# Kernel tuning notes

Hardware: AMD Instinct MI355X
Metric: run time of the kernel (lower is better)

## Reference

```python
import jax, jax.numpy as jnp
import numpy as np

B, C_IN, H, W = 32, 128, 64, 64
C_OUT, K, STRIDE, PAD = 128, 3, 1, 1
M, G = 2, 2
RC = max(C_IN // 16, 16)          # reduction channels = 16
MO = M * C_OUT                    # 256
GRP = G * C_OUT                   # fc groups = 256
OPG = (C_OUT * C_IN * K * K) // GRP   # 576 outputs per fc group
IPG = MO // GRP                   # 1 input per fc group
EPS = 1e-5


def setup_inputs() -> dict:
    key = jax.random.key(0)
    ks = jax.random.split(key, 12)
    s = 0.02
    return {
        "x": jax.random.normal(ks[0], (B, C_IN, H, W), jnp.float32),
        "mask_w": jax.random.normal(ks[1], (1, C_IN), jnp.float32) * s,
        "mask_b": jnp.zeros((1,), jnp.float32),
        "t1_w": jax.random.normal(ks[2], (RC, C_IN), jnp.float32) * s,
        "t1_b": jnp.zeros((RC,), jnp.float32),
        "ln_g": jnp.ones((RC,), jnp.float32),
        "ln_b": jnp.zeros((RC,), jnp.float32),
        "t2_w": jax.random.normal(ks[3], (MO, RC), jnp.float32) * s,
        "t2_b": jnp.zeros((MO,), jnp.float32),
        "fc_w": jax.random.normal(ks[4], (GRP, OPG, IPG), jnp.float32) * s,
        "fc_b": jnp.zeros((GRP * OPG,), jnp.float32),
    }


def reference(x, mask_w, mask_b, t1_w, t1_b, ln_g, ln_b, t2_w, t2_b, fc_w, fc_b):
    b, c, h, w = x.shape
    # --- GC attention context pooling ---
    logits = jnp.einsum('bchw,oc->bohw', x, mask_w) + mask_b[None, :, None, None]
    attn = jax.nn.softmax(logits.reshape(b, h * w), axis=-1)  # [b, hw]
    context = jnp.einsum('bchw,bs->bc', x, attn.reshape(b, h * w)) if False else \
        jnp.einsum('bcs,bs->bc', x.reshape(b, c, h * w), attn)
    # --- transform: conv1x1 -> LayerNorm -> ReLU -> conv1x1 ---
    t = jnp.einsum('bc,rc->br', context, t1_w) + t1_b
    mu = jnp.mean(t, axis=-1, keepdims=True)
    var = jnp.mean((t - mu) ** 2, axis=-1, keepdims=True)
    t = (t - mu) * jax.lax.rsqrt(var + EPS) * ln_g + ln_b
    t = jax.nn.relu(t)
    xw = jnp.einsum('br,or->bo', t, t2_w) + t2_b          # [b, M*out]
    xw = jax.nn.sigmoid(xw)
    # --- grouped 1x1 fc: generates per-sample conv weights ---
    xg = xw.reshape(b, GRP, IPG)
    gen = jnp.einsum('goi,bgi->bgo', fc_w, xg) + fc_b.reshape(GRP, OPG)
    w_gen = gen.reshape(b, C_OUT, C_IN, K, K)             # per-sample kernels
    # --- per-sample conv (groups=b trick in torch) ---
    def conv_one(xi, wi):
        return jax.lax.conv_general_dilated(
            xi[None], wi, (STRIDE, STRIDE), [(PAD, PAD), (PAD, PAD)],
            dimension_numbers=('NCHW', 'OIHW', 'NCHW'))[0]
    out = jax.vmap(conv_one)(x, w_gen)                    # [b, out, h, w]
    return out
```

## Files before the change

### kernel.cpp

```cpp
#include <hip/hip_runtime.h>
#include <hip/hip_bf16.h>

typedef unsigned short u16;
typedef unsigned int u32;
typedef __attribute__((ext_vector_type(8))) short bf16x8;
typedef __attribute__((ext_vector_type(16))) float f32x16;
typedef __attribute__((ext_vector_type(4))) int int4v;
typedef __attribute__((ext_vector_type(4))) float f32x4;

#define CIN 128
#define COUT 128
#define HWSZ 4096
#define RC 16
#define EPS 1e-5f

__device__ __forceinline__ float b2f(u16 u) {
    u32 v = ((u32)u) << 16;
    union { u32 i; float f; } c; c.i = v; return c.f;
}

__device__ __forceinline__ void dma16(const void* g, void* l) {
    __builtin_amdgcn_global_load_lds((const __attribute__((address_space(1))) void*)g,
                                     (__attribute__((address_space(3))) void*)l, 16, 0, 0);
}

__global__ __launch_bounds__(256) void k_xform(const float* __restrict__ x,
                                               const float* __restrict__ mask_w,
                                               const float* __restrict__ mask_b,
                                               u16* __restrict__ xT,
                                               float* __restrict__ attn) {
    int y = blockIdx.x, b = blockIdx.y, t = threadIdx.x;
    __shared__ float tile[128 * 65];
    __shared__ float red[256];

    int c4 = t & 15, ci0 = t >> 4;
#pragma unroll
    for (int i = 0; i < 8; ++i) {
        int ci = ci0 + i * 16;
        f32x4 v = *(const f32x4*)(x + (size_t)(b * 128 + ci) * 4096 + y * 64 + c4 * 4);
        float* tr = tile + ci * 65 + c4 * 4;
        tr[0] = v.x; tr[1] = v.y; tr[2] = v.z; tr[3] = v.w;
    }
    __syncthreads();

    {
        int xs = t & 63, grp = t >> 6;
        float a = 0.f;
#pragma unroll 8
        for (int ci = grp * 32; ci < grp * 32 + 32; ++ci)
            a = fmaf(tile[ci * 65 + xs], mask_w[ci], a);
        red[grp * 64 + xs] = a;
    }

    {
        int xs = t >> 2, q = t & 3;
        u16* dst = xT + ((size_t)b * 4096 + y * 64 + xs) * 128;
        int sw = xs & 7;
#pragma unroll
        for (int k = 0; k < 4; ++k) {
            int cd = q * 4 + k;
            int cs = cd ^ sw;
            u16 tmp[8];
#pragma unroll
            for (int e = 0; e < 8; ++e) {
                __hip_bfloat16 h = __float2bfloat16(tile[(cd * 8 + e) * 65 + xs]);
                tmp[e] = *reinterpret_cast<u16*>(&h);
            }
            *(int4v*)(dst + cs * 8) = *(int4v*)tmp;
        }
    }
    __syncthreads();
    if (t < 64)
        attn[b * HWSZ + y * 64 + t] =
            red[t] + red[64 + t] + red[128 + t] + red[192 + t] + mask_b[0];
}

__global__ __launch_bounds__(256) void k_softmax(float* __restrict__ attn,
                                                 float* __restrict__ ctx) {
    int b = blockIdx.x, t = threadIdx.x;
    if (t < 128) ctx[b * 128 + t] = 0.f;
    float* row = attn + b * HWSZ;
    float v[16];
    float m = -1e30f;
#pragma unroll
    for (int i = 0; i < 16; ++i) { v[i] = row[t + i * 256]; m = fmaxf(m, v[i]); }
    __shared__ float red[256];
    red[t] = m;
    __syncthreads();
    for (int off = 128; off > 0; off >>= 1) {
        if (t < off) red[t] = fmaxf(red[t], red[t + off]);
        __syncthreads();
    }
    m = red[0];
    __syncthreads();
    float s = 0.f;
#pragma unroll
    for (int i = 0; i < 16; ++i) { v[i] = __expf(v[i] - m); s += v[i]; }
    red[t] = s;
    __syncthreads();
    for (int off = 128; off > 0; off >>= 1) {
        if (t < off) red[t] += red[t + off];
        __syncthreads();
    }
    float inv = 1.f / red[0];
#pragma unroll
    for (int i = 0; i < 16; ++i) row[t + i * 256] = v[i] * inv;
}

__global__ __launch_bounds__(256) void k_context(const u16* __restrict__ xT,
                                                 const float* __restrict__ attn,
                                                 float* __restrict__ ctx) {
    int bid = blockIdx.x;
    int b = bid >> 4, sc = bid & 15;
    int t = threadIdx.x, w = t >> 6, l = t & 63;
    const char* xb = (const char*)(xT + (size_t)b * HWSZ * 128);
    float a0 = 0.f, a1 = 0.f;
    int s0 = sc * 256 + w * 64;
    for (int j = 0; j < 64; ++j) {
        int s = s0 + j;
        float av = attn[b * HWSZ + s];
        u32 p = *(const u32*)(xb + (size_t)s * 256 + ((l << 2) ^ ((s & 7) << 4)));
        a0 = fmaf(av, b2f((u16)(p & 0xffff)), a0);
        a1 = fmaf(av, b2f((u16)(p >> 16)), a1);
    }
    __shared__ float red[4][128];
    red[w][2 * l] = a0;
    red[w][2 * l + 1] = a1;
    __syncthreads();
    if (t < 128)
        atomicAdd(&ctx[b * 128 + t], red[0][t] + red[1][t] + red[2][t] + red[3][t]);
}

__global__ __launch_bounds__(256) void k_transform(const float* __restrict__ ctx,
                                                   const float* __restrict__ t1_w,
                                                   const float* __restrict__ t1_b,
                                                   const float* __restrict__ ln_g,
                                                   const float* __restrict__ ln_b,
                                                   const float* __restrict__ t2_w,
                                                   const float* __restrict__ t2_b,
                                                   float* __restrict__ gates) {
    int b = blockIdx.x, t = threadIdx.x;
    __shared__ float c_sh[CIN];
    __shared__ float t_sh[RC];
    if (t < CIN) c_sh[t] = ctx[b * CIN + t];
    __syncthreads();
    if (t < RC) {
        float a = 0.f;
        for (int c = 0; c < CIN; ++c) a = fmaf(c_sh[c], t1_w[t * CIN + c], a);
        t_sh[t] = a + t1_b[t];
    }
    __syncthreads();
    float tv[RC], mu = 0.f;
#pragma unroll
    for (int r = 0; r < RC; ++r) { tv[r] = t_sh[r]; mu += tv[r]; }
    mu *= (1.f / RC);
    float var = 0.f;
#pragma unroll
    for (int r = 0; r < RC; ++r) { float d = tv[r] - mu; var = fmaf(d, d, var); }
    var *= (1.f / RC);
    float rs = rsqrtf(var + EPS);
    float xw = 0.f;
#pragma unroll
    for (int r = 0; r < RC; ++r) {
        float a = fmaxf(0.f, fmaf((tv[r] - mu) * rs, ln_g[r], ln_b[r]));
        xw = fmaf(a, t2_w[t * RC + r], xw);
    }
    xw += t2_b[t];
    gates[b * 256 + t] = 1.f / (1.f + __expf(-xw));
}

__global__ __launch_bounds__(256) void k_genw(const float* __restrict__ fc_w,
                                              const float* __restrict__ fc_b,
                                              const float* __restrict__ gates,
                                              u16* __restrict__ wgen) {
    int bid = blockIdx.x;
    int b = bid >> 6, c = bid & 63;
    int t = threadIdx.x;
    int i = c * 256 + t;
    int co = i >> 7, ci = i & 127;
    float gate = gates[b * 256 + 2 * co + (ci >> 6)];
    int flat = co * 1152 + ci * 9;
    int elem = (((co << 8) | (ci << 1)) ^ ((co & 7) << 4)) >> 1;
    u16* wb = wgen + (size_t)b * 9 * 16384;
#pragma unroll
    for (int p = 0; p < 9; ++p) {
        float v = fmaf(fc_w[flat + p], gate, fc_b[flat + p]);
        __hip_bfloat16 h = __float2bfloat16(v);
        wb[p * 16384 + elem] = *reinterpret_cast<u16*>(&h);
    }
}

__global__ __launch_bounds__(256, 2) void k_conv(const u16* __restrict__ xT,
                                                 const u16* __restrict__ wgen,
                                                 float* __restrict__ out) {
    __shared__ __align__(16) u16 At[16384];
    __shared__ __align__(16) u16 Bt[132 * 128];

    int bid0 = blockIdx.x;
    int xcd = bid0 & 7, i5 = bid0 >> 3;
    int b = xcd * 4 + (i5 >> 5);
    int yp = i5 & 31, y0 = yp * 2;

    int t = threadIdx.x;
    int lane = t & 63, w = t >> 6;
    int wr = w >> 1, wc = w & 1;
    int l31 = lane & 31, l5 = lane >> 5;

    const char* xb = (const char*)(xT + (size_t)b * HWSZ * 128);
    const char* wbase = (const char*)(wgen + (size_t)b * 9 * 16384);

    f32x16 acc00 = {0}, acc01 = {0}, acc10 = {0}, acc11 = {0};

    for (int kh = 0; kh < 3; ++kh) {
        __syncthreads();
        for (int r = 0; r < 2; ++r) {
            int y = y0 + r + kh - 1;
            char* base = (char*)Bt + (r * 66) * 256;
            if ((unsigned)y < 64u) {
                const char* src = xb + (size_t)y * 64 * 256;
#pragma unroll
                for (int i = 0; i < 4; ++i) {
                    int off = (w * 4 + i) * 1024;
                    dma16(src + off + lane * 16, base + 256 + off);
                }
                if (t < 32) {
                    int hr = (t >> 4) * 65;
                    *(int4v*)(base + hr * 256 + (t & 15) * 16) = int4v{0, 0, 0, 0};
                }
            } else {
                for (int i = t; i < 1056; i += 256)
                    *(int4v*)(base + i * 16) = int4v{0, 0, 0, 0};
            }
        }
        for (int kw = 0; kw < 3; ++kw) {
            if (kw) __syncthreads();
            {
                const char* src = wbase + (kh * 3 + kw) * 32768;
                char* dstb = (char*)At;
#pragma unroll
                for (int i = 0; i < 8; ++i) {
                    int off = (w * 8 + i) * 1024;
                    dma16(src + off + lane * 16, dstb + off);
                }
            }
            __syncthreads();
            int rowA0 = wr * 64 + l31, rowA1 = rowA0 + 32;
            int rowB0 = wc * 66 + l31 + kw, rowB1 = rowB0 + 32;
            int sA0 = (rowA0 & 7) << 4, sA1 = (rowA1 & 7) << 4;
            int sB = ((l31 + kw - 1) & 7) << 4;
            const char* Ab = (const char*)At;
            const char* Bb = (const char*)Bt;
#pragma unroll
            for (int ks = 0; ks < 8; ++ks) {
                int kb = ks * 32 + l5 * 16;
                bf16x8 a0 = *(const bf16x8*)(Ab + ((rowA0 << 8) | (kb ^ sA0)));
                bf16x8 a1 = *(const bf16x8*)(Ab + ((rowA1 << 8) | (kb ^ sA1)));
                bf16x8 b0 = *(const bf16x8*)(Bb + ((rowB0 << 8) | (kb ^ sB)));
                bf16x8 b1 = *(const bf16x8*)(Bb + ((rowB1 << 8) | (kb ^ sB)));
                acc00 = __builtin_amdgcn_mfma_f32_32x32x16_bf16(a0, b0, acc00, 0, 0, 0);
                acc01 = __builtin_amdgcn_mfma_f32_32x32x16_bf16(a0, b1, acc01, 0, 0, 0);
                acc10 = __builtin_amdgcn_mfma_f32_32x32x16_bf16(a1, b0, acc10, 0, 0, 0);
                acc11 = __builtin_amdgcn_mfma_f32_32x32x16_bf16(a1, b1, acc11, 0, 0, 0);
            }
        }
    }

    float* ob = out + (size_t)b * COUT * HWSZ;
    int y = y0 + wc;
    auto store_acc = [&](const f32x16& v, int m2, int n4) {
        float* colp = ob + (size_t)(wr * 64 + m2 * 32) * HWSZ + y * 64 + n4 * 32 + l31;
#pragma unroll
        for (int r = 0; r < 16; ++r) {
            int row32 = (r & 3) + ((r >> 2) << 3) + (l5 << 2);
            colp[(size_t)row32 * HWSZ] = v[r];
        }
    };
    store_acc(acc00, 0, 0);
    store_acc(acc01, 0, 1);
    store_acc(acc10, 1, 0);
    store_acc(acc11, 1, 1);
}

extern "C" void kernel_launch(void* const* d_in, const int* in_sizes, int n_in,
                              void* d_out, int out_size, void* d_ws, size_t ws_size,
                              hipStream_t stream) {
    const float* x      = (const float*)d_in[0];
    const float* mask_w = (const float*)d_in[1];
    const float* mask_b = (const float*)d_in[2];
    const float* t1_w   = (const float*)d_in[3];
    const float* t1_b   = (const float*)d_in[4];
    const float* ln_g   = (const float*)d_in[5];
    const float* ln_b   = (const float*)d_in[6];
    const float* t2_w   = (const float*)d_in[7];
    const float* t2_b   = (const float*)d_in[8];
    const float* fc_w   = (const float*)d_in[9];
    const float* fc_b   = (const float*)d_in[10];
    float* out = (float*)d_out;

    char* ws = (char*)d_ws;
    u16*   xT    = (u16*)ws;
    float* attn  = (float*)(ws + 33554432);
    float* ctx   = (float*)(ws + 34078720);
    float* gates = (float*)(ws + 34095104);
    u16*   wgen  = (u16*)(ws + 34127872);

    k_xform    <<<dim3(64, 32), 256, 0, stream>>>(x, mask_w, mask_b, xT, attn);
    k_softmax  <<<32,  256, 0, stream>>>(attn, ctx);
    k_context  <<<512, 256, 0, stream>>>(xT, attn, ctx);
    k_transform<<<32,  256, 0, stream>>>(ctx, t1_w, t1_b, ln_g, ln_b, t2_w, t2_b, gates);
    k_genw     <<<2048, 256, 0, stream>>>(fc_w, fc_b, gates, wgen);
    k_conv     <<<1024, 256, 0, stream>>>(xT, wgen, out);
}
```

Before: 200.8 us.

## Fuse softmax and transform stages, register-prefetch conv weights from global memory

The separate softmax kernel is removed. k_xform now writes unnormalized exp logits and atomically accumulates a per-sample sum, and k_context divides by that sum and uses 16-byte vector loads. The transform MLP is fused into k_genw, which now uses vectorized fc loads and writes the generated weights in a per-lane fragment layout. k_conv drops the LDS staging of weights and instead double-buffers A fragments in registers loaded straight from global memory, which removes the per-kw barriers. The exp without max subtraction can overflow for large logits, and the extra registers may pressure occupancy.

```diff
diff --git a/kernel.cpp b/kernel.cpp
--- a/kernel.cpp
+++ b/kernel.cpp
@@ -28,7 +28,8 @@
                                                const float* __restrict__ mask_w,
                                                const float* __restrict__ mask_b,
                                                u16* __restrict__ xT,
-                                               float* __restrict__ attn) {
+                                               float* __restrict__ attn,
+                                               float* __restrict__ sumexp) {
     int y = blockIdx.x, b = blockIdx.y, t = threadIdx.x;
     __shared__ float tile[128 * 65];
     __shared__ float red[256];
@@ -70,130 +71,123 @@
         }
     }
     __syncthreads();
-    if (t < 64)
-        attn[b * HWSZ + y * 64 + t] =
-            red[t] + red[64 + t] + red[128 + t] + red[192 + t] + mask_b[0];
-}
-
-__global__ __launch_bounds__(256) void k_softmax(float* __restrict__ attn,
-                                                 float* __restrict__ ctx) {
-    int b = blockIdx.x, t = threadIdx.x;
-    if (t < 128) ctx[b * 128 + t] = 0.f;
-    float* row = attn + b * HWSZ;
-    float v[16];
-    float m = -1e30f;
-#pragma unroll
-    for (int i = 0; i < 16; ++i) { v[i] = row[t + i * 256]; m = fmaxf(m, v[i]); }
-    __shared__ float red[256];
-    red[t] = m;
-    __syncthreads();
-    for (int off = 128; off > 0; off >>= 1) {
-        if (t < off) red[t] = fmaxf(red[t], red[t + off]);
-        __syncthreads();
-    }
-    m = red[0];
-    __syncthreads();
-    float s = 0.f;
-#pragma unroll
-    for (int i = 0; i < 16; ++i) { v[i] = __expf(v[i] - m); s += v[i]; }
-    red[t] = s;
-    __syncthreads();
-    for (int off = 128; off > 0; off >>= 1) {
-        if (t < off) red[t] += red[t + off];
-        __syncthreads();
-    }
-    float inv = 1.f / red[0];
-#pragma unroll
-    for (int i = 0; i < 16; ++i) row[t + i * 256] = v[i] * inv;
+    if (t < 64) {
+        float e = __expf(red[t] + red[64 + t] + red[128 + t] + red[192 + t] + mask_b[0]);
+        attn[b * HWSZ + y * 64 + t] = e;
+        float s = e;
+#pragma unroll
+        for (int off = 32; off; off >>= 1) s += __shfl_down(s, off);
+        if (t == 0) atomicAdd(&sumexp[b], s);
+    }
 }
 
 __global__ __launch_bounds__(256) void k_context(const u16* __restrict__ xT,
                                                  const float* __restrict__ attn,
+                                                 const float* __restrict__ sumexp,
                                                  float* __restrict__ ctx) {
     int bid = blockIdx.x;
     int b = bid >> 4, sc = bid & 15;
-    int t = threadIdx.x, w = t >> 6, l = t & 63;
+    int t = threadIdx.x;
+    int px = t >> 4, cg = t & 15;
     const char* xb = (const char*)(xT + (size_t)b * HWSZ * 128);
-    float a0 = 0.f, a1 = 0.f;
-    int s0 = sc * 256 + w * 64;
-    for (int j = 0; j < 64; ++j) {
-        int s = s0 + j;
-        float av = attn[b * HWSZ + s];
-        u32 p = *(const u32*)(xb + (size_t)s * 256 + ((l << 2) ^ ((s & 7) << 4)));
-        a0 = fmaf(av, b2f((u16)(p & 0xffff)), a0);
-        a1 = fmaf(av, b2f((u16)(p >> 16)), a1);
-    }
-    __shared__ float red[4][128];
-    red[w][2 * l] = a0;
-    red[w][2 * l + 1] = a1;
-    __syncthreads();
-    if (t < 128)
-        atomicAdd(&ctx[b * 128 + t], red[0][t] + red[1][t] + red[2][t] + red[3][t]);
-}
-
-__global__ __launch_bounds__(256) void k_transform(const float* __restrict__ ctx,
-                                                   const float* __restrict__ t1_w,
-                                                   const float* __restrict__ t1_b,
-                                                   const float* __restrict__ ln_g,
-                                                   const float* __restrict__ ln_b,
-                                                   const float* __restrict__ t2_w,
-                                                   const float* __restrict__ t2_b,
-                                                   float* __restrict__ gates) {
-    int b = blockIdx.x, t = threadIdx.x;
-    __shared__ float c_sh[CIN];
-    __shared__ float t_sh[RC];
-    if (t < CIN) c_sh[t] = ctx[b * CIN + t];
+    float acc[8] = {0.f, 0.f, 0.f, 0.f, 0.f, 0.f, 0.f, 0.f};
+    int s0 = sc * 256 + px;
+    int coff = (cg * 16) ^ ((px & 7) << 4);
+    for (int j = 0; j < 16; ++j) {
+        int s = s0 + j * 16;
+        float e = attn[b * HWSZ + s];
+        int4v u = *(const int4v*)(xb + (size_t)s * 256 + coff);
+        const u16* q = (const u16*)&u;
+#pragma unroll
+        for (int k = 0; k < 8; ++k) acc[k] = fmaf(e, b2f(q[k]), acc[k]);
+    }
+    __shared__ float red[16][132];
+#pragma unroll
+    for (int k = 0; k < 8; ++k) red[px][cg * 8 + k] = acc[k];
+    __syncthreads();
+    if (t < 128) {
+        float s = 0.f;
+#pragma unroll
+        for (int g = 0; g < 16; ++g) s += red[g][t];
+        atomicAdd(&ctx[b * 128 + t], s / sumexp[b]);
+    }
+}
+
+__global__ __launch_bounds__(256) void k_genw(const float* __restrict__ ctx,
+                                              const float* __restrict__ t1_w,
+                                              const float* __restrict__ t1_b,
+                                              const float* __restrict__ ln_g,
+                                              const float* __restrict__ ln_b,
+                                              const float* __restrict__ t2_w,
+                                              const float* __restrict__ t2_b,
+                                              const float* __restrict__ fc_w,
+                                              const float* __restrict__ fc_b,
+                                              u16* __restrict__ wgen) {
+    int bid = blockIdx.x;
+    int b = bid >> 3, g = bid & 7;
+    int t = threadIdx.x;
+    __shared__ float ctx_sh[128];
+    __shared__ float traw[RC];
+    __shared__ float gate_sh[64];
+    if (t < 128) ctx_sh[t] = ctx[b * 128 + t];
     __syncthreads();
     if (t < RC) {
         float a = 0.f;
-        for (int c = 0; c < CIN; ++c) a = fmaf(c_sh[c], t1_w[t * CIN + c], a);
-        t_sh[t] = a + t1_b[t];
-    }
-    __syncthreads();
-    float tv[RC], mu = 0.f;
-#pragma unroll
-    for (int r = 0; r < RC; ++r) { tv[r] = t_sh[r]; mu += tv[r]; }
-    mu *= (1.f / RC);
-    float var = 0.f;
-#pragma unroll
-    for (int r = 0; r < RC; ++r) { float d = tv[r] - mu; var = fmaf(d, d, var); }
-    var *= (1.f / RC);
-    float rs = rsqrtf(var + EPS);
-    float xw = 0.f;
-#pragma unroll
-    for (int r = 0; r < RC; ++r) {
-        float a = fmaxf(0.f, fmaf((tv[r] - mu) * rs, ln_g[r], ln_b[r]));
-        xw = fmaf(a, t2_w[t * RC + r], xw);
-    }
-    xw += t2_b[t];
-    gates[b * 256 + t] = 1.f / (1.f + __expf(-xw));
-}
-
-__global__ __launch_bounds__(256) void k_genw(const float* __restrict__ fc_w,
-                                              const float* __restrict__ fc_b,
-                                              const float* __restrict__ gates,
-                                              u16* __restrict__ wgen) {
-    int bid = blockIdx.x;
-    int b = bid >> 6, c = bid & 63;
-    int t = threadIdx.x;
-    int i = c * 256 + t;
-    int co = i >> 7, ci = i & 127;
-    float gate = gates[b * 256 + 2 * co + (ci >> 6)];
-    int flat = co * 1152 + ci * 9;
-    int elem = (((co << 8) | (ci << 1)) ^ ((co & 7) << 4)) >> 1;
+        for (int c = 0; c < 128; ++c) a = fmaf(ctx_sh[c], t1_w[t * 128 + c], a);
+        traw[t] = a + t1_b[t];
+    }
+    __syncthreads();
+    int r32g = g >> 1;
+    if (t < 64) {
+        float tv[RC], mu = 0.f;
+#pragma unroll
+        for (int r = 0; r < RC; ++r) { tv[r] = traw[r]; mu += tv[r]; }
+        mu *= (1.f / RC);
+        float var = 0.f;
+#pragma unroll
+        for (int r = 0; r < RC; ++r) { float d = tv[r] - mu; var = fmaf(d, d, var); }
+        var *= (1.f / RC);
+        float rs = rsqrtf(var + EPS);
+        int gi = r32g * 64 + t;
+        float xw = 0.f;
+#pragma unroll
+        for (int r = 0; r < RC; ++r) {
+            float a = fmaxf(0.f, fmaf((tv[r] - mu) * rs, ln_g[r], ln_b[r]));
+            xw = fmaf(a, t2_w[gi * RC + r], xw);
+        }
+        xw += t2_b[gi];
+        gate_sh[t] = 1.f / (1.f + __expf(-xw));
+    }
+    __syncthreads();
+    int U = g * 256 + t;
+    int r32 = U >> 9, c = (U >> 5) & 15, l31 = U & 31;
+    int co = r32 * 32 + l31;
+    float gate = gate_sh[l31 * 2 + (c >> 3)];
+    int base = co * 1152 + c * 72;
+    float wv[72], bv[72];
+#pragma unroll
+    for (int i = 0; i < 18; ++i) {
+        *(f32x4*)&wv[i * 4] = *(const f32x4*)(fc_w + base + i * 4);
+        *(f32x4*)&bv[i * 4] = *(const f32x4*)(fc_b + base + i * 4);
+    }
     u16* wb = wgen + (size_t)b * 9 * 16384;
+    int unit = r32 * 512 + c * 32 + l31;
 #pragma unroll
     for (int p = 0; p < 9; ++p) {
-        float v = fmaf(fc_w[flat + p], gate, fc_b[flat + p]);
-        __hip_bfloat16 h = __float2bfloat16(v);
-        wb[p * 16384 + elem] = *reinterpret_cast<u16*>(&h);
+        u16 tmp[8];
+#pragma unroll
+        for (int e = 0; e < 8; ++e) {
+            float v = fmaf(wv[e * 9 + p], gate, bv[e * 9 + p]);
+            __hip_bfloat16 h = __float2bfloat16(v);
+            tmp[e] = *reinterpret_cast<u16*>(&h);
+        }
+        *(int4v*)(wb + p * 16384 + unit * 8) = *(int4v*)tmp;
     }
 }
 
 __global__ __launch_bounds__(256, 2) void k_conv(const u16* __restrict__ xT,
                                                  const u16* __restrict__ wgen,
                                                  float* __restrict__ out) {
-    __shared__ __align__(16) u16 At[16384];
     __shared__ __align__(16) u16 Bt[132 * 128];
 
     int bid0 = blockIdx.x;
@@ -208,61 +202,73 @@
 
     const char* xb = (const char*)(xT + (size_t)b * HWSZ * 128);
     const char* wbase = (const char*)(wgen + (size_t)b * 9 * 16384);
-
+    const char* abase = wbase + wr * 16384 + l5 * 512 + l31 * 16;
+
+    bf16x8 RA[16], RB[16];
     f32x16 acc00 = {0}, acc01 = {0}, acc10 = {0}, acc11 = {0};
-
-    for (int kh = 0; kh < 3; ++kh) {
-        __syncthreads();
-        for (int r = 0; r < 2; ++r) {
-            int y = y0 + r + kh - 1;
-            char* base = (char*)Bt + (r * 66) * 256;
-            if ((unsigned)y < 64u) {
-                const char* src = xb + (size_t)y * 64 * 256;
-#pragma unroll
-                for (int i = 0; i < 4; ++i) {
-                    int off = (w * 4 + i) * 1024;
-                    dma16(src + off + lane * 16, base + 256 + off);
-                }
-                if (t < 32) {
-                    int hr = (t >> 4) * 65;
-                    *(int4v*)(base + hr * 256 + (t & 15) * 16) = int4v{0, 0, 0, 0};
-                }
-            } else {
-                for (int i = t; i < 1056; i += 256)
-                    *(int4v*)(base + i * 16) = int4v{0, 0, 0, 0};
-            }
-        }
-        for (int kw = 0; kw < 3; ++kw) {
-            if (kw) __syncthreads();
-            {
-                const char* src = wbase + (kh * 3 + kw) * 32768;
-                char* dstb = (char*)At;
-#pragma unroll
-                for (int i = 0; i < 8; ++i) {
-                    int off = (w * 8 + i) * 1024;
-                    dma16(src + off + lane * 16, dstb + off);
-                }
-            }
+    const char* Bb = (const char*)Bt;
+    int rowB0 = wc * 66 + l31;
+
+#define LOADP(P, R)                                                        \
+    {                                                                      \
+        const char* ap = abase + (P) * 32768;                              \
+        _Pragma("unroll") for (int ks = 0; ks < 8; ++ks) {                 \
+            R[ks]     = *(const bf16x8*)(ap + ks * 1024);                  \
+            R[8 + ks] = *(const bf16x8*)(ap + 8192 + ks * 1024);           \
+        }                                                                  \
+    }
+
+#define COMPUTE(P, R)                                                              \
+    {                                                                              \
+        const int kw = (P) % 3;                                                    \
+        int rB0 = (rowB0 + kw) << 8;                                               \
+        int rB1 = rB0 + (32 << 8);                                                 \
+        int sB = ((l31 + kw - 1) & 7) << 4;                                        \
+        _Pragma("unroll") for (int ks = 0; ks < 8; ++ks) {                         \
+            int kb = ks * 32 + l5 * 16;                                            \
+            bf16x8 b0 = *(const bf16x8*)(Bb + (rB0 | (kb ^ sB)));                  \
+            bf16x8 b1 = *(const bf16x8*)(Bb + (rB1 | (kb ^ sB)));                  \
+            acc00 = __builtin_amdgcn_mfma_f32_32x32x16_bf16(R[ks], b0, acc00, 0, 0, 0);     \
+            acc01 = __builtin_amdgcn_mfma_f32_32x32x16_bf16(R[ks], b1, acc01, 0, 0, 0);     \
+            acc10 = __builtin_amdgcn_mfma_f32_32x32x16_bf16(R[8 + ks], b0, acc10, 0, 0, 0); \
+            acc11 = __builtin_amdgcn_mfma_f32_32x32x16_bf16(R[8 + ks], b1, acc11, 0, 0, 0); \
+        }                                                                          \
+    }
+
+#define STAGEB(KH)                                                                   \
+    {                                                                                \
+        _Pragma("unroll") for (int r = 0; r < 2; ++r) {                              \
+            int y = y0 + r + (KH) - 1;                                               \
+            char* base = (char*)Bt + (r * 66) * 256;                                 \
+            if ((unsigned)y < 64u) {                                                 \
+                const char* src = xb + (size_t)y * 64 * 256;                         \
+                _Pragma("unroll") for (int i = 0; i < 4; ++i) {                      \
+                    int off = (w * 4 + i) * 1024;                                    \
+                    dma16(src + off + lane * 16, base + 256 + off);                  \
+                }                                                                    \
+                if (t < 32) {                                                        \
+                    int hr = (t >> 4) * 65;                                          \
+                    *(int4v*)(base + hr * 256 + (t & 15) * 16) = int4v{0, 0, 0, 0};  \
+                }                                                                    \
+            } else {                                                                 \
+                for (int i = t; i < 1056; i += 256)                                  \
+                    *(int4v*)(base + i * 16) = int4v{0, 0, 0, 0};                    \
+            }                                                                        \
+        }                                                                            \
+    }
+
+    LOADP(0, RA);
+#pragma unroll
+    for (int p = 0; p < 9; ++p) {
+        if (p % 3 == 0) {
             __syncthreads();
-            int rowA0 = wr * 64 + l31, rowA1 = rowA0 + 32;
-            int rowB0 = wc * 66 + l31 + kw, rowB1 = rowB0 + 32;
-            int sA0 = (rowA0 & 7) << 4, sA1 = (rowA1 & 7) << 4;
-            int sB = ((l31 + kw - 1) & 7) << 4;
-            const char* Ab = (const char*)At;
-            const char* Bb = (const char*)Bt;
-#pragma unroll
-            for (int ks = 0; ks < 8; ++ks) {
-                int kb = ks * 32 + l5 * 16;
-                bf16x8 a0 = *(const bf16x8*)(Ab + ((rowA0 << 8) | (kb ^ sA0)));
-                bf16x8 a1 = *(const bf16x8*)(Ab + ((rowA1 << 8) | (kb ^ sA1)));
-                bf16x8 b0 = *(const bf16x8*)(Bb + ((rowB0 << 8) | (kb ^ sB)));
-                bf16x8 b1 = *(const bf16x8*)(Bb + ((rowB1 << 8) | (kb ^ sB)));
-                acc00 = __builtin_amdgcn_mfma_f32_32x32x16_bf16(a0, b0, acc00, 0, 0, 0);
-                acc01 = __builtin_amdgcn_mfma_f32_32x32x16_bf16(a0, b1, acc01, 0, 0, 0);
-                acc10 = __builtin_amdgcn_mfma_f32_32x32x16_bf16(a1, b0, acc10, 0, 0, 0);
-                acc11 = __builtin_amdgcn_mfma_f32_32x32x16_bf16(a1, b1, acc11, 0, 0, 0);
-            }
-        }
+            STAGEB(p / 3);
+            __syncthreads();
+        }
+        if (p < 8) {
+            if (p & 1) { LOADP(p + 1, RA); } else { LOADP(p + 1, RB); }
+        }
+        if (p & 1) { COMPUTE(p, RB); } else { COMPUTE(p, RA); }
     }
 
     float* ob = out + (size_t)b * COUT * HWSZ;
@@ -279,6 +285,9 @@
     store_acc(acc01, 0, 1);
     store_acc(acc10, 1, 0);
     store_acc(acc11, 1, 1);
+#undef LOADP
+#undef COMPUTE
+#undef STAGEB
 }
 
 extern "C" void kernel_launch(void* const* d_in, const int* in_sizes, int n_in,
@@ -298,16 +307,17 @@
     float* out = (float*)d_out;
 
     char* ws = (char*)d_ws;
-    u16*   xT    = (u16*)ws;
-    float* attn  = (float*)(ws + 33554432);
-    float* ctx   = (float*)(ws + 34078720);
-    float* gates = (float*)(ws + 34095104);
-    u16*   wgen  = (u16*)(ws + 34127872);
-
-    k_xform    <<<dim3(64, 32), 256, 0, stream>>>(x, mask_w, mask_b, xT, attn);
-    k_softmax  <<<32,  256, 0, stream>>>(attn, ctx);
-    k_context  <<<512, 256, 0, stream>>>(xT, attn, ctx);
-    k_transform<<<32,  256, 0, stream>>>(ctx, t1_w, t1_b, ln_g, ln_b, t2_w, t2_b, gates);
-    k_genw     <<<2048, 256, 0, stream>>>(fc_w, fc_b, gates, wgen);
-    k_conv     <<<1024, 256, 0, stream>>>(xT, wgen, out);
-}
+    u16*   xT     = (u16*)ws;
+    float* attn   = (float*)(ws + 33554432);
+    float* ctx    = (float*)(ws + 34078720);
+    float* sumexp = (float*)(ws + 34095104);
+    u16*   wgen   = (u16*)(ws + 34096128);
+
+    hipMemsetAsync(ws + 34078720, 0, 17408, stream);
+
+    k_xform  <<<dim3(64, 32), 256, 0, stream>>>(x, mask_w, mask_b, xT, attn, sumexp);
+    k_context<<<512, 256, 0, stream>>>(xT, attn, sumexp, ctx);
+    k_genw   <<<256, 256, 0, stream>>>(ctx, t1_w, t1_b, ln_g, ln_b,
+                                       t2_w, t2_b, fc_w, fc_b, wgen);
+    k_conv   <<<1024, 256, 0, stream>>>(xT, wgen, out);
+}
```

After: 215.5 us. 7.3% more time.
